# Kernel tuning notes

Hardware: AMD Instinct MI355X
Metric: run time of the kernel (lower is better)

The kernel has to match this reference:

```python
import jax, jax.numpy as jnp
import numpy as np

HIDDEN = 2048
N_HEADS = 32
N_KV_HEADS = 8
HEAD_DIM = HIDDEN // N_HEADS  # 64
KV_GROUPS = N_HEADS // N_KV_HEADS  # 4
ROPE_THETA = 10000.0
BSZ, SEQ = 2, 2048


def setup_inputs() -> dict:
    key = jax.random.key(0)
    ks = jax.random.split(key, 5)
    s = 0.02
    hidden_states = jax.random.normal(ks[0], (BSZ, SEQ, HIDDEN), jnp.float32)
    position_ids = jnp.broadcast_to(jnp.arange(SEQ, dtype=jnp.int32), (BSZ, SEQ))
    Wq = jax.random.normal(ks[1], (HIDDEN, HIDDEN), jnp.float32) * s
    Wk = jax.random.normal(ks[2], (N_KV_HEADS * HEAD_DIM, HIDDEN), jnp.float32) * s
    Wv = jax.random.normal(ks[3], (N_KV_HEADS * HEAD_DIM, HIDDEN), jnp.float32) * s
    Wo = jax.random.normal(ks[4], (HIDDEN, HIDDEN), jnp.float32) * s
    return {"hidden_states": hidden_states, "position_ids": position_ids,
            "Wq": Wq, "Wk": Wk, "Wv": Wv, "Wo": Wo}


def _rope_cos_sin(position_ids):
    # Llama rotary embedding: inv_freq over even dims, emb = [freqs, freqs]
    inv_freq = 1.0 / (ROPE_THETA ** (jnp.arange(0, HEAD_DIM, 2, dtype=jnp.float32) / HEAD_DIM))  # [Hd/2]
    freqs = position_ids.astype(jnp.float32)[..., None] * inv_freq  # [B, S, Hd/2]
    emb = jnp.concatenate([freqs, freqs], axis=-1)  # [B, S, Hd]
    return jnp.cos(emb), jnp.sin(emb)


def _rotate_half(x):
    x1, x2 = jnp.split(x, 2, axis=-1)
    return jnp.concatenate([-x2, x1], axis=-1)


def reference(hidden_states, position_ids, Wq, Wk, Wv, Wo):
    bsz, seq_len, _ = hidden_states.shape
    # projections (nn.Linear: y = x @ W.T)
    q = (hidden_states @ Wq.T).reshape(bsz, seq_len, N_HEADS, HEAD_DIM).transpose(0, 2, 1, 3)
    k = (hidden_states @ Wk.T).reshape(bsz, seq_len, N_KV_HEADS, HEAD_DIM).transpose(0, 2, 1, 3)
    v = (hidden_states @ Wv.T).reshape(bsz, seq_len, N_KV_HEADS, HEAD_DIM).transpose(0, 2, 1, 3)
    cos, sin = _rope_cos_sin(position_ids)  # [B, S, Hd]
    cos = cos[:, None, :, :]
    sin = sin[:, None, :, :]
    q = q * cos + _rotate_half(q) * sin
    k = k * cos + _rotate_half(k) * sin
    # GQA expand kv heads to full head count
    k = jnp.repeat(k, KV_GROUPS, axis=1)  # [B, H, S, Hd]
    v = jnp.repeat(v, KV_GROUPS, axis=1)
    # naive full-softmax attention (no causal mask, matching the source)
    scores = jnp.einsum('bhqd,bhkd->bhqk', q, k) / jnp.sqrt(jnp.float32(HEAD_DIM))
    attn_w = jax.nn.softmax(scores, axis=-1)
    attn_o = jnp.einsum('bhqk,bhkd->bhqd', attn_w, v)
    attn_o = attn_o.transpose(0, 2, 1, 3).reshape(bsz, seq_len, HIDDEN)
    return attn_o @ Wo.T
```

## Files before the change

### kernel.cpp

```cpp
#include <hip/hip_runtime.h>
#include <hip/hip_bf16.h>
#include <stdint.h>

#define HID 2048
#define NH 32
#define NKV 8
#define HD 64
#define BSZ 2
#define SEQ 2048
#define NROWS (BSZ*SEQ)
#define KVCOLS (NKV*HD)
#define QKVN 3072

typedef __attribute__((ext_vector_type(8))) short bf16x8;
typedef __attribute__((ext_vector_type(4))) float f32x4;
typedef __attribute__((ext_vector_type(16))) float f32x16;
typedef __attribute__((ext_vector_type(2))) unsigned int u32x2;

__device__ __forceinline__ unsigned short f2bf(float f) {
  union { float f; uint32_t u; } v; v.f = f;
  uint32_t r = v.u + 0x7FFFu + ((v.u >> 16) & 1u);
  return (unsigned short)(r >> 16);
}

__device__ __forceinline__ unsigned pack_bf16(float a, float b) {
  union { __hip_bfloat162 h; unsigned u; } cv;
  cv.h = __float22bfloat162_rn(make_float2(a, b));
  return cv.u;
}

__device__ __forceinline__ float sum16(const f32x16& s) {
  float a0 = s[0] + s[1], a1 = s[2] + s[3], a2 = s[4] + s[5], a3 = s[6] + s[7];
  float a4 = s[8] + s[9], a5 = s[10] + s[11], a6 = s[12] + s[13], a7 = s[14] + s[15];
  float b0 = a0 + a1, b1 = a2 + a3, b2 = a4 + a5, b3 = a6 + a7;
  return (b0 + b1) + (b2 + b3);
}

#define MKPB(S, B0) ({ \
  unsigned A_ = pack_bf16((S)[B0], (S)[(B0)+1]); \
  unsigned C_ = pack_bf16((S)[(B0)+2], (S)[(B0)+3]); \
  unsigned B_ = pack_bf16((S)[(B0)+4], (S)[(B0)+5]); \
  unsigned D_ = pack_bf16((S)[(B0)+6], (S)[(B0)+7]); \
  u32x2 r0_ = __builtin_amdgcn_permlane32_swap(A_, B_, false, false); \
  u32x2 r1_ = __builtin_amdgcn_permlane32_swap(C_, D_, false, false); \
  union { uint4 u; bf16x8 v; } cv_; \
  cv_.u.x = r0_.x; cv_.u.y = r1_.x; cv_.u.z = r0_.y; cv_.u.w = r1_.y; \
  cv_.v; })

__global__ __launch_bounds__(256) void cvt_kernel(const float* __restrict__ in,
                                                  unsigned short* __restrict__ out, int n) {
  int idx = (blockIdx.x * 256 + threadIdx.x) * 4;
  int stride = gridDim.x * 256 * 4;
  for (int i = idx; i < n; i += stride) {
    float4 v = *(const float4*)(in + i);
    ushort4 o;
    o.x = f2bf(v.x); o.y = f2bf(v.y); o.z = f2bf(v.z); o.w = f2bf(v.w);
    *(ushort4*)(out + i) = o;
  }
}

#define BM 128
#define BN 128
#define BK 32

__global__ __launch_bounds__(256) void gemm_btn(
    const unsigned short* __restrict__ A,
    const unsigned short* __restrict__ B,
    float* __restrict__ C,
    int M, int N, int K)
{
  __shared__ unsigned short As[2][BM * BK];
  __shared__ unsigned short Bs[2][BN * BK];
  const int t = threadIdx.x;
  const int w = t >> 6, l = t & 63;
  const int wr = w >> 1, wc = w & 1;
  const int row0 = blockIdx.y * BM, col0 = blockIdx.x * BN;
  const int lr = l & 15, lk = (l >> 4) * 8;

  f32x4 acc[4][4];
  for (int i = 0; i < 4; ++i)
    for (int j = 0; j < 4; ++j)
      acc[i][j] = (f32x4){0.f, 0.f, 0.f, 0.f};

  auto stage = [&](int bi, int k0) {
    #pragma unroll
    for (int i = 0; i < 2; ++i) {
      int ebase = i * 2048 + w * 512;
      int e = ebase + l * 8;
      const unsigned short* srcA = A + (size_t)(row0 + (e >> 5)) * K + k0 + (e & 31);
      const unsigned short* srcB = B + (size_t)(col0 + (e >> 5)) * K + k0 + (e & 31);
      __builtin_amdgcn_global_load_lds((const __attribute__((address_space(1))) void*)srcA,
          (__attribute__((address_space(3))) void*)&As[bi][ebase], 16, 0, 0);
      __builtin_amdgcn_global_load_lds((const __attribute__((address_space(1))) void*)srcB,
          (__attribute__((address_space(3))) void*)&Bs[bi][ebase], 16, 0, 0);
    }
  };

  stage(0, 0);
  __syncthreads();
  int bi = 0;
  for (int k0 = 0; k0 < K; k0 += BK) {
    if (k0 + BK < K) stage(bi ^ 1, k0 + BK);
    bf16x8 a[4], b[4];
    #pragma unroll
    for (int mi = 0; mi < 4; ++mi)
      a[mi] = *(const bf16x8*)&As[bi][(wr * 64 + mi * 16 + lr) * BK + lk];
    #pragma unroll
    for (int ni = 0; ni < 4; ++ni)
      b[ni] = *(const bf16x8*)&Bs[bi][(wc * 64 + ni * 16 + lr) * BK + lk];
    #pragma unroll
    for (int mi = 0; mi < 4; ++mi)
      #pragma unroll
      for (int ni = 0; ni < 4; ++ni)
        acc[mi][ni] = __builtin_amdgcn_mfma_f32_16x16x32_bf16(a[mi], b[ni], acc[mi][ni], 0, 0, 0);
    __syncthreads();
    bi ^= 1;
  }

  const int crow = (l >> 4) * 4, ccol = l & 15;
  #pragma unroll
  for (int mi = 0; mi < 4; ++mi)
    #pragma unroll
    for (int ni = 0; ni < 4; ++ni) {
      float* cp = C + (size_t)(row0 + wr * 64 + mi * 16 + crow) * N + col0 + wc * 64 + ni * 16 + ccol;
      #pragma unroll
      for (int r = 0; r < 4; ++r)
        cp[(size_t)r * N] = acc[mi][ni][r];
    }
}

__global__ __launch_bounds__(256) void rope_k_kernel(const float* __restrict__ QKVf,
                                                     const int* __restrict__ pos_ids,
                                                     unsigned short* __restrict__ Kb) {
  int row = blockIdx.x;
  int t = threadIdx.x;
  int kh = t >> 5, j = t & 31;
  int b = row >> 11, s = row & 2047;
  float pos = (float)pos_ids[row];
  float invf = exp2f((float)j * -0.41524101186092029f);
  float sn, c;
  __sincosf(pos * invf, &sn, &c);
  const float* kr = QKVf + (size_t)row * QKVN + HID + kh * 64;
  float k1 = kr[j], k2 = kr[j + 32];
  float o1 = k1 * c - k2 * sn;
  float o2 = k2 * c + k1 * sn;
  unsigned short* outp = Kb + ((size_t)(b * NKV + kh) * SEQ + s) * HD;
  outp[j] = f2bf(o1);
  outp[j + 32] = f2bf(o2);
}

__global__ __launch_bounds__(256) void vt_kernel(const float* __restrict__ QKVf,
                                                 unsigned short* __restrict__ Vt) {
  int bid = blockIdx.x;
  int stile = bid & 31;
  int kh = (bid >> 5) & 7;
  int b = bid >> 8;
  int s0 = stile * 64;
  __shared__ unsigned short Ts[64][65];
  int t = threadIdx.x;
  {
    int r = t >> 2;
    int dq = (t & 3) * 16;
    const float* src = QKVf + (size_t)(b * SEQ + s0 + r) * QKVN + (HID + KVCOLS) + kh * 64 + dq;
    #pragma unroll
    for (int i = 0; i < 4; ++i) {
      float4 v = *(const float4*)(src + i * 4);
      Ts[r][dq + i * 4 + 0] = f2bf(v.x);
      Ts[r][dq + i * 4 + 1] = f2bf(v.y);
      Ts[r][dq + i * 4 + 2] = f2bf(v.z);
      Ts[r][dq + i * 4 + 3] = f2bf(v.w);
    }
  }
  __syncthreads();
  {
    int d = t >> 2;
    int cb = (t & 3) * 16;
    unsigned short* dst = Vt + ((size_t)(b * NKV + kh) * 64 + d) * SEQ + s0 + cb;
    #pragma unroll
    for (int i = 0; i < 4; ++i) {
      ushort4 o;
      o.x = Ts[cb + i * 4 + 0][d];
      o.y = Ts[cb + i * 4 + 1][d];
      o.z = Ts[cb + i * 4 + 2][d];
      o.w = Ts[cb + i * 4 + 3][d];
      *(ushort4*)(dst + i * 4) = o;
    }
  }
}

__global__ __launch_bounds__(256, 2) void attn_kernel(
    const float* __restrict__ QKVf,
    const int* __restrict__ pos_ids,
    const unsigned short* __restrict__ Kb,
    const unsigned short* __restrict__ Vt,
    unsigned short* __restrict__ AO)
{
  __shared__ unsigned short Ks[2][128 * 64];
  __shared__ unsigned short Vs[2][2][64 * 64];

  const int bid = blockIdx.x;
  const int qtile = bid & 15;
  const int h = (bid >> 4) & 31;
  const int b = bid >> 9;
  const int kh = h >> 2;
  const int t = threadIdx.x, w = t >> 6, l = t & 63;
  const int lq = l & 31, hi = l >> 5;
  const int sw = (lq & 7) << 4;
  const int qrow = qtile * 128 + w * 32 + lq;

  bf16x8 qf[4];
  {
    const float SCL = 0.18033688011112042f;
    const float* Qsrc = QKVf + (size_t)(b * SEQ + qrow) * QKVN + h * 64;
    float pos = (float)pos_ids[b * SEQ + qrow];
    #pragma unroll
    for (int dk = 0; dk < 2; ++dk) {
      float4 a0 = *(const float4*)(Qsrc + dk * 16 + hi * 8);
      float4 a1 = *(const float4*)(Qsrc + dk * 16 + hi * 8 + 4);
      float4 b0 = *(const float4*)(Qsrc + 32 + dk * 16 + hi * 8);
      float4 b1 = *(const float4*)(Qsrc + 32 + dk * 16 + hi * 8 + 4);
      float x1[8] = {a0.x, a0.y, a0.z, a0.w, a1.x, a1.y, a1.z, a1.w};
      float x2[8] = {b0.x, b0.y, b0.z, b0.w, b1.x, b1.y, b1.z, b1.w};
      union { bf16x8 v; unsigned short us[8]; } lov, hiv;
      #pragma unroll
      for (int jj = 0; jj < 8; ++jj) {
        float jidx = (float)(dk * 16 + hi * 8 + jj);
        float sn, cs;
        __sincosf(pos * exp2f(jidx * -0.41524101186092029f), &sn, &cs);
        lov.us[jj] = f2bf((x1[jj] * cs - x2[jj] * sn) * SCL);
        hiv.us[jj] = f2bf((x2[jj] * cs + x1[jj] * sn) * SCL);
      }
      qf[dk] = lov.v;
      qf[dk + 2] = hiv.v;
    }
  }

  const unsigned short* Kt  = Kb + (size_t)(b * NKV + kh) * SEQ * HD;
  const unsigned short* Vth = Vt + (size_t)(b * NKV + kh) * HD * SEQ;

  auto stage = [&](int si, int kv0) {
    #pragma unroll
    for (int r = 0; r < 4; ++r) {
      int dest = r * 4096 + t * 16;
      int row = dest >> 7;
      int xsw = (row & 7) << 4;
      const char* Ksrc = (const char*)(Kt + (size_t)kv0 * HD) + (dest ^ xsw);
      __builtin_amdgcn_global_load_lds((const __attribute__((address_space(1))) void*)Ksrc,
          (__attribute__((address_space(3))) void*)((char*)&Ks[si][0] + dest), 16, 0, 0);
    }
    #pragma unroll
    for (int c = 0; c < 2; ++c)
      #pragma unroll
      for (int r = 0; r < 2; ++r) {
        int dest = r * 4096 + t * 16;
        int row = dest >> 7;
        int col = dest & 127;
        int xsw = (row & 7) << 4;
        const char* Vsrc = (const char*)(Vth + (size_t)row * SEQ + kv0 + c * 64) + (col ^ xsw);
        __builtin_amdgcn_global_load_lds((const __attribute__((address_space(1))) void*)Vsrc,
            (__attribute__((address_space(3))) void*)((char*)&Vs[si][c][0] + dest), 16, 0, 0);
      }
  };

  const f32x16 Z = {0,0,0,0,0,0,0,0,0,0,0,0,0,0,0,0};
  float lsum = 0.f;
  f32x16 o0 = Z, o1 = Z;

  stage(0, 0);

  int bi = 0;
  for (int it = 0; it < SEQ / 128; ++it) {
    if (it + 1 < SEQ / 128) {
      stage(bi ^ 1, (it + 1) * 128);
      asm volatile("s_waitcnt vmcnt(8)" ::: "memory");
    } else {
      asm volatile("s_waitcnt vmcnt(0)" ::: "memory");
    }
    __builtin_amdgcn_s_barrier();
    __builtin_amdgcn_sched_barrier(0);

    #pragma unroll
    for (int c = 0; c < 2; ++c) {
      const char* Kp = (const char*)&Ks[bi][0] + c * 8192;
      const char* Vp = (const char*)&Vs[bi][c][0];

      f32x16 s0, s1;
      __builtin_amdgcn_s_setprio(1);
      {
        bf16x8 kf0 = *(const bf16x8*)(Kp + lq * 128 + ((hi * 16) ^ sw));
        bf16x8 kf1 = *(const bf16x8*)(Kp + 4096 + lq * 128 + ((hi * 16) ^ sw));
        s0 = __builtin_amdgcn_mfma_f32_32x32x16_bf16(kf0, qf[0], Z, 0, 0, 0);
        s1 = __builtin_amdgcn_mfma_f32_32x32x16_bf16(kf1, qf[0], Z, 0, 0, 0);
      }
      #pragma unroll
      for (int dk = 1; dk < 4; ++dk) {
        const int cb = dk * 32 + hi * 16;
        bf16x8 kf0 = *(const bf16x8*)(Kp + lq * 128 + (cb ^ sw));
        bf16x8 kf1 = *(const bf16x8*)(Kp + 4096 + lq * 128 + (cb ^ sw));
        s0 = __builtin_amdgcn_mfma_f32_32x32x16_bf16(kf0, qf[dk], s0, 0, 0, 0);
        s1 = __builtin_amdgcn_mfma_f32_32x32x16_bf16(kf1, qf[dk], s1, 0, 0, 0);
      }
      __builtin_amdgcn_s_setprio(0);

      #pragma unroll
      for (int r = 0; r < 16; ++r) { s0[r] = exp2f(s0[r]); s1[r] = exp2f(s1[r]); }
      float rs = sum16(s0) + sum16(s1);
      rs += __shfl_xor(rs, 32);
      lsum += rs;

      bf16x8 pb0 = MKPB(s0, 0), pb1 = MKPB(s0, 8), pb2 = MKPB(s1, 0), pb3 = MKPB(s1, 8);

      __builtin_amdgcn_s_setprio(1);
      #pragma unroll
      for (int ks = 0; ks < 4; ++ks) {
        const int cb = ks * 32 + hi * 16;
        bf16x8 vf0 = *(const bf16x8*)(Vp + lq * 128 + (cb ^ sw));
        bf16x8 vf1 = *(const bf16x8*)(Vp + 4096 + lq * 128 + (cb ^ sw));
        bf16x8 pa = (ks == 0) ? pb0 : (ks == 1) ? pb1 : (ks == 2) ? pb2 : pb3;
        o0 = __builtin_amdgcn_mfma_f32_32x32x16_bf16(vf0, pa, o0, 0, 0, 0);
        o1 = __builtin_amdgcn_mfma_f32_32x32x16_bf16(vf1, pa, o1, 0, 0, 0);
      }
      __builtin_amdgcn_s_setprio(0);
    }

    __builtin_amdgcn_sched_barrier(0);
    __builtin_amdgcn_s_barrier();
    bi ^= 1;
  }

  const float inv = 1.0f / lsum;
  unsigned short* op = AO + ((size_t)(b * SEQ) + qrow) * HID + h * 64;
  #pragma unroll
  for (int r = 0; r < 16; r += 2) {
    const int d = (r & 3) + 8 * (r >> 2) + 4 * hi;
    *(unsigned*)(op + d)      = pack_bf16(o0[r] * inv, o0[r + 1] * inv);
    *(unsigned*)(op + 32 + d) = pack_bf16(o1[r] * inv, o1[r + 1] * inv);
  }
}

extern "C" void kernel_launch(void* const* d_in, const int* in_sizes, int n_in,
                              void* d_out, int out_size, void* d_ws, size_t ws_size,
                              hipStream_t stream) {
  const float* hs  = (const float*)d_in[0];
  const int*   pos = (const int*)d_in[1];
  const float* Wq  = (const float*)d_in[2];
  const float* Wk  = (const float*)d_in[3];
  const float* Wv  = (const float*)d_in[4];
  const float* Wo  = (const float*)d_in[5];
  float* out = (float*)d_out;

  char* ws = (char*)d_ws;
  size_t off = 0;
  auto carve = [&](size_t bytes) { void* p = ws + off; off += (bytes + 255) & ~(size_t)255; return p; };

  unsigned short* Xb    = (unsigned short*)carve((size_t)NROWS * HID * 2);
  unsigned short* Wqkvb = (unsigned short*)carve((size_t)QKVN * HID * 2);
  unsigned short* Wob   = (unsigned short*)carve((size_t)HID * HID * 2);
  float*          QKVf  = (float*)carve((size_t)NROWS * QKVN * 4);
  unsigned short* Kbh   = (unsigned short*)carve((size_t)NROWS * KVCOLS * 2);
  unsigned short* Vtb   = (unsigned short*)carve((size_t)NROWS * KVCOLS * 2);
  unsigned short* AO    = (unsigned short*)carve((size_t)NROWS * HID * 2);

  cvt_kernel<<<1024, 256, 0, stream>>>(hs, Xb, NROWS * HID);
  cvt_kernel<<<512, 256, 0, stream>>>(Wq, Wqkvb, HID * HID);
  cvt_kernel<<<256, 256, 0, stream>>>(Wk, Wqkvb + (size_t)HID * HID, KVCOLS * HID);
  cvt_kernel<<<256, 256, 0, stream>>>(Wv, Wqkvb + (size_t)(HID + KVCOLS) * HID, KVCOLS * HID);
  cvt_kernel<<<512, 256, 0, stream>>>(Wo, Wob, HID * HID);

  gemm_btn<<<dim3(QKVN / BN, NROWS / BM), 256, 0, stream>>>(Xb, Wqkvb, QKVf, NROWS, QKVN, HID);

  rope_k_kernel<<<NROWS, 256, 0, stream>>>(QKVf, pos, Kbh);
  vt_kernel<<<BSZ * NKV * (SEQ / 64), 256, 0, stream>>>(QKVf, Vtb);

  attn_kernel<<<BSZ * NH * (SEQ / 128), 256, 0, stream>>>(QKVf, pos, Kbh, Vtb, AO);

  gemm_btn<<<dim3(HID / BN, NROWS / BM), 256, 0, stream>>>(AO, Wob, out, NROWS, HID, HID);
}
```

Measured before the change: 271.8 us.

## Load K/V fragments directly from global memory instead of LDS staging

The attention kernel drops its double-buffered LDS staging of K and V tiles, which used global_load_lds with barriers. Each wave now loads its MFMA operand fragments straight from global memory into registers, one 64-key block per iteration. Launch bounds are raised to 4 blocks per SM. This removes LDS traffic and block-wide barriers, but K/V reuse across the 4 waves now depends on L1/L2 caches. There is no explicit prefetch, so global load latency is only hidden by occupancy.

```diff
diff --git a/kernel.cpp b/kernel.cpp
--- a/kernel.cpp
+++ b/kernel.cpp
@@ -188,16 +188,13 @@
   }
 }
 
-__global__ __launch_bounds__(256, 2) void attn_kernel(
+__global__ __launch_bounds__(256, 4) void attn_kernel(
     const float* __restrict__ QKVf,
     const int* __restrict__ pos_ids,
     const unsigned short* __restrict__ Kb,
     const unsigned short* __restrict__ Vt,
     unsigned short* __restrict__ AO)
 {
-  __shared__ unsigned short Ks[2][128 * 64];
-  __shared__ unsigned short Vs[2][2][64 * 64];
-
   const int bid = blockIdx.x;
   const int qtile = bid & 15;
   const int h = (bid >> 4) & 31;
@@ -205,7 +202,6 @@
   const int kh = h >> 2;
   const int t = threadIdx.x, w = t >> 6, l = t & 63;
   const int lq = l & 31, hi = l >> 5;
-  const int sw = (lq & 7) << 4;
   const int qrow = qtile * 128 + w * 32 + lq;
 
   bf16x8 qf[4];
@@ -235,97 +231,59 @@
     }
   }
 
-  const unsigned short* Kt  = Kb + (size_t)(b * NKV + kh) * SEQ * HD;
-  const unsigned short* Vth = Vt + (size_t)(b * NKV + kh) * HD * SEQ;
-
-  auto stage = [&](int si, int kv0) {
-    #pragma unroll
-    for (int r = 0; r < 4; ++r) {
-      int dest = r * 4096 + t * 16;
-      int row = dest >> 7;
-      int xsw = (row & 7) << 4;
-      const char* Ksrc = (const char*)(Kt + (size_t)kv0 * HD) + (dest ^ xsw);
-      __builtin_amdgcn_global_load_lds((const __attribute__((address_space(1))) void*)Ksrc,
-          (__attribute__((address_space(3))) void*)((char*)&Ks[si][0] + dest), 16, 0, 0);
-    }
-    #pragma unroll
-    for (int c = 0; c < 2; ++c)
-      #pragma unroll
-      for (int r = 0; r < 2; ++r) {
-        int dest = r * 4096 + t * 16;
-        int row = dest >> 7;
-        int col = dest & 127;
-        int xsw = (row & 7) << 4;
-        const char* Vsrc = (const char*)(Vth + (size_t)row * SEQ + kv0 + c * 64) + (col ^ xsw);
-        __builtin_amdgcn_global_load_lds((const __attribute__((address_space(1))) void*)Vsrc,
-            (__attribute__((address_space(3))) void*)((char*)&Vs[si][c][0] + dest), 16, 0, 0);
-      }
-  };
+  const unsigned short* kp = Kb + (size_t)(b * NKV + kh) * SEQ * HD + lq * 64 + hi * 8;
+  const unsigned short* vp0 = Vt + (size_t)(b * NKV + kh) * HD * SEQ + (size_t)lq * SEQ + hi * 8;
+  const unsigned short* vp1 = vp0 + 32 * SEQ;
 
   const f32x16 Z = {0,0,0,0,0,0,0,0,0,0,0,0,0,0,0,0};
   float lsum = 0.f;
   f32x16 o0 = Z, o1 = Z;
 
-  stage(0, 0);
-
-  int bi = 0;
-  for (int it = 0; it < SEQ / 128; ++it) {
-    if (it + 1 < SEQ / 128) {
-      stage(bi ^ 1, (it + 1) * 128);
-      asm volatile("s_waitcnt vmcnt(8)" ::: "memory");
-    } else {
-      asm volatile("s_waitcnt vmcnt(0)" ::: "memory");
-    }
-    __builtin_amdgcn_s_barrier();
-    __builtin_amdgcn_sched_barrier(0);
-
-    #pragma unroll
-    for (int c = 0; c < 2; ++c) {
-      const char* Kp = (const char*)&Ks[bi][0] + c * 8192;
-      const char* Vp = (const char*)&Vs[bi][c][0];
-
-      f32x16 s0, s1;
-      __builtin_amdgcn_s_setprio(1);
-      {
-        bf16x8 kf0 = *(const bf16x8*)(Kp + lq * 128 + ((hi * 16) ^ sw));
-        bf16x8 kf1 = *(const bf16x8*)(Kp + 4096 + lq * 128 + ((hi * 16) ^ sw));
-        s0 = __builtin_amdgcn_mfma_f32_32x32x16_bf16(kf0, qf[0], Z, 0, 0, 0);
-        s1 = __builtin_amdgcn_mfma_f32_32x32x16_bf16(kf1, qf[0], Z, 0, 0, 0);
-      }
-      #pragma unroll
-      for (int dk = 1; dk < 4; ++dk) {
-        const int cb = dk * 32 + hi * 16;
-        bf16x8 kf0 = *(const bf16x8*)(Kp + lq * 128 + (cb ^ sw));
-        bf16x8 kf1 = *(const bf16x8*)(Kp + 4096 + lq * 128 + (cb ^ sw));
-        s0 = __builtin_amdgcn_mfma_f32_32x32x16_bf16(kf0, qf[dk], s0, 0, 0, 0);
-        s1 = __builtin_amdgcn_mfma_f32_32x32x16_bf16(kf1, qf[dk], s1, 0, 0, 0);
-      }
-      __builtin_amdgcn_s_setprio(0);
-
-      #pragma unroll
-      for (int r = 0; r < 16; ++r) { s0[r] = exp2f(s0[r]); s1[r] = exp2f(s1[r]); }
-      float rs = sum16(s0) + sum16(s1);
-      rs += __shfl_xor(rs, 32);
-      lsum += rs;
-
-      bf16x8 pb0 = MKPB(s0, 0), pb1 = MKPB(s0, 8), pb2 = MKPB(s1, 0), pb3 = MKPB(s1, 8);
-
-      __builtin_amdgcn_s_setprio(1);
-      #pragma unroll
-      for (int ks = 0; ks < 4; ++ks) {
-        const int cb = ks * 32 + hi * 16;
-        bf16x8 vf0 = *(const bf16x8*)(Vp + lq * 128 + (cb ^ sw));
-        bf16x8 vf1 = *(const bf16x8*)(Vp + 4096 + lq * 128 + (cb ^ sw));
-        bf16x8 pa = (ks == 0) ? pb0 : (ks == 1) ? pb1 : (ks == 2) ? pb2 : pb3;
-        o0 = __builtin_amdgcn_mfma_f32_32x32x16_bf16(vf0, pa, o0, 0, 0, 0);
-        o1 = __builtin_amdgcn_mfma_f32_32x32x16_bf16(vf1, pa, o1, 0, 0, 0);
-      }
-      __builtin_amdgcn_s_setprio(0);
-    }
-
-    __builtin_amdgcn_sched_barrier(0);
-    __builtin_amdgcn_s_barrier();
-    bi ^= 1;
+  for (int it = 0; it < SEQ / 64; ++it) {
+    bf16x8 kf0[4], kf1[4];
+    #pragma unroll
+    for (int dk = 0; dk < 4; ++dk) {
+      kf0[dk] = *(const bf16x8*)(kp + dk * 16);
+      kf1[dk] = *(const bf16x8*)(kp + 2048 + dk * 16);
+    }
+    bf16x8 vf0[4], vf1[4];
+    #pragma unroll
+    for (int ks = 0; ks < 4; ++ks) {
+      vf0[ks] = *(const bf16x8*)(vp0 + ks * 16);
+      vf1[ks] = *(const bf16x8*)(vp1 + ks * 16);
+    }
+
+    f32x16 s0, s1;
+    __builtin_amdgcn_s_setprio(1);
+    s0 = __builtin_amdgcn_mfma_f32_32x32x16_bf16(kf0[0], qf[0], Z, 0, 0, 0);
+    s1 = __builtin_amdgcn_mfma_f32_32x32x16_bf16(kf1[0], qf[0], Z, 0, 0, 0);
+    #pragma unroll
+    for (int dk = 1; dk < 4; ++dk) {
+      s0 = __builtin_amdgcn_mfma_f32_32x32x16_bf16(kf0[dk], qf[dk], s0, 0, 0, 0);
+      s1 = __builtin_amdgcn_mfma_f32_32x32x16_bf16(kf1[dk], qf[dk], s1, 0, 0, 0);
+    }
+    __builtin_amdgcn_s_setprio(0);
+
+    #pragma unroll
+    for (int r = 0; r < 16; ++r) { s0[r] = exp2f(s0[r]); s1[r] = exp2f(s1[r]); }
+    float rs = sum16(s0) + sum16(s1);
+    rs += __shfl_xor(rs, 32);
+    lsum += rs;
+
+    bf16x8 pb0 = MKPB(s0, 0), pb1 = MKPB(s0, 8), pb2 = MKPB(s1, 0), pb3 = MKPB(s1, 8);
+
+    __builtin_amdgcn_s_setprio(1);
+    #pragma unroll
+    for (int ks = 0; ks < 4; ++ks) {
+      bf16x8 pa = (ks == 0) ? pb0 : (ks == 1) ? pb1 : (ks == 2) ? pb2 : pb3;
+      o0 = __builtin_amdgcn_mfma_f32_32x32x16_bf16(vf0[ks], pa, o0, 0, 0, 0);
+      o1 = __builtin_amdgcn_mfma_f32_32x32x16_bf16(vf1[ks], pa, o1, 0, 0, 0);
+    }
+    __builtin_amdgcn_s_setprio(0);
+
+    kp += 64 * 64;
+    vp0 += 64;
+    vp1 += 64;
   }
 
   const float inv = 1.0f / lsum;
```

Result: slower. 455.4 us (+67.5%).

## Enlarge attention workgroups to 256 queries, register-staged KV, and swizzle block order

Applied to the files above, without the earlier changes.

The attention kernel now uses 512-thread workgroups covering 256 query rows, so each K/V tile loaded into LDS is shared by twice as many queries. The KV tile shrinks to 64 keys and is staged through registers with a double-buffered LDS write in place of direct global-to-LDS loads. Block indices in both the GEMM and attention kernels are remapped in groups of 8, likely so that consecutive blocks spread across XCDs or share a KV head for better L2 locality. The trade-off is more barriers per KV step and more register pressure from the 4-waves-per-SIMD launch bound.

```diff
diff --git a/kernel.cpp b/kernel.cpp
--- a/kernel.cpp
+++ b/kernel.cpp
@@ -74,7 +74,13 @@
   const int t = threadIdx.x;
   const int w = t >> 6, l = t & 63;
   const int wr = w >> 1, wc = w & 1;
-  const int row0 = blockIdx.y * BM, col0 = blockIdx.x * BN;
+
+  const int nwg = gridDim.x * gridDim.y;
+  const int lin = blockIdx.y * gridDim.x + blockIdx.x;
+  const int swz = (lin & 7) * (nwg >> 3) + (lin >> 3);
+  const int bx = swz % gridDim.x, by = swz / gridDim.x;
+
+  const int row0 = by * BM, col0 = bx * BN;
   const int lr = l & 15, lk = (l >> 4) * 8;
 
   f32x4 acc[4][4];
@@ -188,25 +194,26 @@
   }
 }
 
-__global__ __launch_bounds__(256, 2) void attn_kernel(
+__global__ __launch_bounds__(512, 4) void attn_kernel(
     const float* __restrict__ QKVf,
     const int* __restrict__ pos_ids,
     const unsigned short* __restrict__ Kb,
     const unsigned short* __restrict__ Vt,
     unsigned short* __restrict__ AO)
 {
-  __shared__ unsigned short Ks[2][128 * 64];
-  __shared__ unsigned short Vs[2][2][64 * 64];
-
-  const int bid = blockIdx.x;
-  const int qtile = bid & 15;
-  const int h = (bid >> 4) & 31;
-  const int b = bid >> 9;
+  __shared__ unsigned short Ks[2][64 * 64];
+  __shared__ unsigned short Vs[2][64 * 64];
+
+  const int lin = blockIdx.x;
+  const int bid = (lin & 7) * 64 + (lin >> 3);
+  const int qtile = bid & 7;
+  const int h = (bid >> 3) & 31;
+  const int b = bid >> 8;
   const int kh = h >> 2;
   const int t = threadIdx.x, w = t >> 6, l = t & 63;
   const int lq = l & 31, hi = l >> 5;
   const int sw = (lq & 7) << 4;
-  const int qrow = qtile * 128 + w * 32 + lq;
+  const int qrow = qtile * 256 + w * 32 + lq;
 
   bf16x8 qf[4];
   {
@@ -238,93 +245,79 @@
   const unsigned short* Kt  = Kb + (size_t)(b * NKV + kh) * SEQ * HD;
   const unsigned short* Vth = Vt + (size_t)(b * NKV + kh) * HD * SEQ;
 
-  auto stage = [&](int si, int kv0) {
-    #pragma unroll
-    for (int r = 0; r < 4; ++r) {
-      int dest = r * 4096 + t * 16;
-      int row = dest >> 7;
-      int xsw = (row & 7) << 4;
-      const char* Ksrc = (const char*)(Kt + (size_t)kv0 * HD) + (dest ^ xsw);
-      __builtin_amdgcn_global_load_lds((const __attribute__((address_space(1))) void*)Ksrc,
-          (__attribute__((address_space(3))) void*)((char*)&Ks[si][0] + dest), 16, 0, 0);
-    }
-    #pragma unroll
-    for (int c = 0; c < 2; ++c)
-      #pragma unroll
-      for (int r = 0; r < 2; ++r) {
-        int dest = r * 4096 + t * 16;
-        int row = dest >> 7;
-        int col = dest & 127;
-        int xsw = (row & 7) << 4;
-        const char* Vsrc = (const char*)(Vth + (size_t)row * SEQ + kv0 + c * 64) + (col ^ xsw);
-        __builtin_amdgcn_global_load_lds((const __attribute__((address_space(1))) void*)Vsrc,
-            (__attribute__((address_space(3))) void*)((char*)&Vs[si][c][0] + dest), 16, 0, 0);
-      }
+  const int dest = t * 16;
+  const int srow = dest >> 7;
+  const int scol = dest & 127;
+  const int wdest = dest ^ ((srow & 7) << 4);
+  const char* KsrcBase = (const char*)Kt + dest;
+  const char* VsrcBase = (const char*)(Vth + (size_t)srow * SEQ) + scol;
+
+  uint4 kreg, vreg;
+  auto issue = [&](int kv0) {
+    kreg = *(const uint4*)(KsrcBase + (size_t)kv0 * 128);
+    vreg = *(const uint4*)(VsrcBase + kv0 * 2);
+  };
+  auto lwrite = [&](int si) {
+    *(uint4*)((char*)Ks[si] + wdest) = kreg;
+    *(uint4*)((char*)Vs[si] + wdest) = vreg;
   };
 
   const f32x16 Z = {0,0,0,0,0,0,0,0,0,0,0,0,0,0,0,0};
   float lsum = 0.f;
   f32x16 o0 = Z, o1 = Z;
 
-  stage(0, 0);
+  issue(0);
+  lwrite(0);
+  __syncthreads();
 
   int bi = 0;
-  for (int it = 0; it < SEQ / 128; ++it) {
-    if (it + 1 < SEQ / 128) {
-      stage(bi ^ 1, (it + 1) * 128);
-      asm volatile("s_waitcnt vmcnt(8)" ::: "memory");
-    } else {
-      asm volatile("s_waitcnt vmcnt(0)" ::: "memory");
-    }
-    __builtin_amdgcn_s_barrier();
-    __builtin_amdgcn_sched_barrier(0);
-
-    #pragma unroll
-    for (int c = 0; c < 2; ++c) {
-      const char* Kp = (const char*)&Ks[bi][0] + c * 8192;
-      const char* Vp = (const char*)&Vs[bi][c][0];
-
-      f32x16 s0, s1;
-      __builtin_amdgcn_s_setprio(1);
-      {
-        bf16x8 kf0 = *(const bf16x8*)(Kp + lq * 128 + ((hi * 16) ^ sw));
-        bf16x8 kf1 = *(const bf16x8*)(Kp + 4096 + lq * 128 + ((hi * 16) ^ sw));
-        s0 = __builtin_amdgcn_mfma_f32_32x32x16_bf16(kf0, qf[0], Z, 0, 0, 0);
-        s1 = __builtin_amdgcn_mfma_f32_32x32x16_bf16(kf1, qf[0], Z, 0, 0, 0);
-      }
-      #pragma unroll
-      for (int dk = 1; dk < 4; ++dk) {
-        const int cb = dk * 32 + hi * 16;
-        bf16x8 kf0 = *(const bf16x8*)(Kp + lq * 128 + (cb ^ sw));
-        bf16x8 kf1 = *(const bf16x8*)(Kp + 4096 + lq * 128 + (cb ^ sw));
-        s0 = __builtin_amdgcn_mfma_f32_32x32x16_bf16(kf0, qf[dk], s0, 0, 0, 0);
-        s1 = __builtin_amdgcn_mfma_f32_32x32x16_bf16(kf1, qf[dk], s1, 0, 0, 0);
-      }
-      __builtin_amdgcn_s_setprio(0);
-
-      #pragma unroll
-      for (int r = 0; r < 16; ++r) { s0[r] = exp2f(s0[r]); s1[r] = exp2f(s1[r]); }
-      float rs = sum16(s0) + sum16(s1);
-      rs += __shfl_xor(rs, 32);
-      lsum += rs;
-
-      bf16x8 pb0 = MKPB(s0, 0), pb1 = MKPB(s0, 8), pb2 = MKPB(s1, 0), pb3 = MKPB(s1, 8);
-
-      __builtin_amdgcn_s_setprio(1);
-      #pragma unroll
-      for (int ks = 0; ks < 4; ++ks) {
-        const int cb = ks * 32 + hi * 16;
-        bf16x8 vf0 = *(const bf16x8*)(Vp + lq * 128 + (cb ^ sw));
-        bf16x8 vf1 = *(const bf16x8*)(Vp + 4096 + lq * 128 + (cb ^ sw));
-        bf16x8 pa = (ks == 0) ? pb0 : (ks == 1) ? pb1 : (ks == 2) ? pb2 : pb3;
-        o0 = __builtin_amdgcn_mfma_f32_32x32x16_bf16(vf0, pa, o0, 0, 0, 0);
-        o1 = __builtin_amdgcn_mfma_f32_32x32x16_bf16(vf1, pa, o1, 0, 0, 0);
-      }
-      __builtin_amdgcn_s_setprio(0);
-    }
-
-    __builtin_amdgcn_sched_barrier(0);
-    __builtin_amdgcn_s_barrier();
+  for (int it = 0; it < SEQ / 64; ++it) {
+    const bool more = (it + 1 < SEQ / 64);
+    if (more) issue((it + 1) * 64);
+
+    const char* Kp = (const char*)Ks[bi];
+    const char* Vp = (const char*)Vs[bi];
+
+    f32x16 s0, s1;
+    __builtin_amdgcn_s_setprio(1);
+    {
+      bf16x8 kf0 = *(const bf16x8*)(Kp + lq * 128 + ((hi * 16) ^ sw));
+      bf16x8 kf1 = *(const bf16x8*)(Kp + 4096 + lq * 128 + ((hi * 16) ^ sw));
+      s0 = __builtin_amdgcn_mfma_f32_32x32x16_bf16(kf0, qf[0], Z, 0, 0, 0);
+      s1 = __builtin_amdgcn_mfma_f32_32x32x16_bf16(kf1, qf[0], Z, 0, 0, 0);
+    }
+    #pragma unroll
+    for (int dk = 1; dk < 4; ++dk) {
+      const int cb = dk * 32 + hi * 16;
+      bf16x8 kf0 = *(const bf16x8*)(Kp + lq * 128 + (cb ^ sw));
+      bf16x8 kf1 = *(const bf16x8*)(Kp + 4096 + lq * 128 + (cb ^ sw));
+      s0 = __builtin_amdgcn_mfma_f32_32x32x16_bf16(kf0, qf[dk], s0, 0, 0, 0);
+      s1 = __builtin_amdgcn_mfma_f32_32x32x16_bf16(kf1, qf[dk], s1, 0, 0, 0);
+    }
+    __builtin_amdgcn_s_setprio(0);
+
+    #pragma unroll
+    for (int r = 0; r < 16; ++r) { s0[r] = exp2f(s0[r]); s1[r] = exp2f(s1[r]); }
+    float rs = sum16(s0) + sum16(s1);
+    rs += __shfl_xor(rs, 32);
+    lsum += rs;
+
+    bf16x8 pb0 = MKPB(s0, 0), pb1 = MKPB(s0, 8), pb2 = MKPB(s1, 0), pb3 = MKPB(s1, 8);
+
+    __builtin_amdgcn_s_setprio(1);
+    #pragma unroll
+    for (int ks = 0; ks < 4; ++ks) {
+      const int cb = ks * 32 + hi * 16;
+      bf16x8 vf0 = *(const bf16x8*)(Vp + lq * 128 + (cb ^ sw));
+      bf16x8 vf1 = *(const bf16x8*)(Vp + 4096 + lq * 128 + (cb ^ sw));
+      bf16x8 pa = (ks == 0) ? pb0 : (ks == 1) ? pb1 : (ks == 2) ? pb2 : pb3;
+      o0 = __builtin_amdgcn_mfma_f32_32x32x16_bf16(vf0, pa, o0, 0, 0, 0);
+      o1 = __builtin_amdgcn_mfma_f32_32x32x16_bf16(vf1, pa, o1, 0, 0, 0);
+    }
+    __builtin_amdgcn_s_setprio(0);
+
+    if (more) lwrite(bi ^ 1);
+    __syncthreads();
     bi ^= 1;
   }
 
@@ -372,7 +365,7 @@
   rope_k_kernel<<<NROWS, 256, 0, stream>>>(QKVf, pos, Kbh);
   vt_kernel<<<BSZ * NKV * (SEQ / 64), 256, 0, stream>>>(QKVf, Vtb);
 
-  attn_kernel<<<BSZ * NH * (SEQ / 128), 256, 0, stream>>>(QKVf, pos, Kbh, Vtb, AO);
+  attn_kernel<<<BSZ * NH * (SEQ / 256), 512, 0, stream>>>(QKVf, pos, Kbh, Vtb, AO);
 
   gemm_btn<<<dim3(HID / BN, NROWS / BM), 256, 0, stream>>>(AO, Wob, out, NROWS, HID, HID);
 }
```

Measured after the change: 256.1 us. 1.06x faster.
